# Kernel optimization log

Measured on AMD Instinct MI355X. Metric: run time of the kernel, lower is better.

Reference implementation:

```python
import jax, jax.numpy as jnp
import numpy as np

N_NODES = 50000
N_EDGES = 800000
D = 64  # node_dim == edge_dim
NEG_SLOPE = 0.2
EPS = 1e-5


def _lin_params(key, d_in, d_out):
    k1, k2 = jax.random.split(key)
    bound = 1.0 / np.sqrt(d_in)
    W = jax.random.uniform(k1, (d_out, d_in), minval=-bound, maxval=bound, dtype=jnp.float32)
    b = jax.random.uniform(k2, (d_out,), minval=-bound, maxval=bound, dtype=jnp.float32)
    return W, b


def setup_inputs() -> dict:
    key = jax.random.key(0)
    ks = jax.random.split(key, 12)
    V = jax.random.normal(ks[0], (N_NODES, D), dtype=jnp.float32)
    E = jax.random.normal(ks[1], (N_EDGES, D), dtype=jnp.float32)
    src = jax.random.randint(ks[2], (N_EDGES,), 0, N_NODES, dtype=jnp.int32)
    dst = jax.random.randint(ks[3], (N_EDGES,), 0, N_NODES, dtype=jnp.int32)
    pA_w, pA_b = _lin_params(ks[4], D, D)   # NodePooling.A
    pB_w, pB_b = _lin_params(ks[5], D, D)   # NodePooling.B
    mW1, mb1 = _lin_params(ks[6], D, D)     # edge MLP layer 1
    mW2, mb2 = _lin_params(ks[7], D, D)     # edge MLP layer 2
    BW, Bb = _lin_params(ks[8], D, D)       # GenMessage.B (scale)
    CW, Cb = _lin_params(ks[9], D, D)       # GenMessage.C (shift)
    return {"V": V, "E": E, "src": src, "dst": dst,
            "pA_w": pA_w, "pA_b": pA_b, "pB_w": pB_w, "pB_b": pB_b,
            "mW1": mW1, "mb1": mb1, "mW2": mW2, "mb2": mb2,
            "BW": BW, "Bb": Bb, "CW": CW, "Cb": Cb}


def _lrelu(x):
    return jnp.where(x >= 0, x, NEG_SLOPE * x)


def reference(V, E, src, dst, pA_w, pA_b, pB_w, pB_b, mW1, mb1, mW2, mb2, BW, Bb, CW, Cb):
    n = V.shape[0]
    # V = act(V); NodePooling: B(lrelu(A(V)))
    Va = _lrelu(V)
    Vp = _lrelu(Va @ pA_w.T + pA_b) @ pB_w.T + pB_b  # [N, D]
    # edge MLP on edge features (2 Linear+ReLU layers)
    x = jax.nn.relu(E @ mW1.T + mb1)
    x = jax.nn.relu(x @ mW2.T + mb2)                  # [E, D]
    scale = jax.nn.sigmoid(x @ BW.T + Bb)
    shift = x @ CW.T + Cb
    # gathered src features, gated affine message
    M1 = scale * Vp[src] + shift                      # [E, D]
    M2 = M1 * M1
    # segment-mean onto dst (DGL fn.mean); zero for isolated nodes
    deg = jax.ops.segment_sum(jnp.ones((dst.shape[0],), jnp.float32), dst, num_segments=n)
    denom = jnp.maximum(deg, 1.0)[:, None]
    V1 = jax.ops.segment_sum(M1, dst, num_segments=n) / denom
    V2 = jax.ops.segment_sum(M2, dst, num_segments=n) / denom
    return jnp.sqrt(jax.nn.relu(V2 - V1) + EPS)
```

## Files before the change

kernel.cpp:

```cpp
#include <hip/hip_runtime.h>

#define NN 50000
#define NE 800000
#define DDIM 64
#define PADX 68
#define PADS 68
#define NB_SCAN ((NN + 255) / 256)
#define NPB ((NN + 63) / 64)
#define NEG_SLOPE 0.2f
#define EPS_V 1e-5f

typedef short bf16x8 __attribute__((ext_vector_type(8)));
typedef float f32x4 __attribute__((ext_vector_type(4)));

__device__ __forceinline__ float lrelu_f(float x) { return x >= 0.0f ? x : NEG_SLOPE * x; }

__device__ __forceinline__ unsigned short bf16_rn(float x) {
    union { float f; unsigned int u; } c; c.f = x;
    unsigned int r = c.u + 0x7FFF + ((c.u >> 16) & 1);
    return (unsigned short)(r >> 16);
}
__device__ __forceinline__ float bf16_tof(unsigned short h) {
    union { float f; unsigned int u; } c; c.u = ((unsigned int)h) << 16;
    return c.f;
}

__device__ __forceinline__ unsigned cvtpk_bf16(float a, float b) {
    unsigned r;
    asm("v_cvt_pk_bf16_f32 %0, %1, %2" : "=v"(r) : "v"(a), "v"(b));
    return r;
}

__device__ __forceinline__ void split8(const float* __restrict__ v, bf16x8& h, bf16x8& l)
{
    union { bf16x8 v8; unsigned u[4]; } H, L;
    #pragma unroll
    for (int k = 0; k < 4; ++k) {
        float a = v[2*k], b = v[2*k+1];
        unsigned p = cvtpk_bf16(a, b);
        union { float f; unsigned u; } h0, h1;
        h0.u = p << 16;
        h1.u = p & 0xFFFF0000u;
        unsigned q = cvtpk_bf16(a - h0.f, b - h1.f);
        H.u[k] = p;
        L.u[k] = q;
    }
    h = H.v8; l = L.v8;
}

__device__ __forceinline__ void mma_tile(float acc[16], const float* __restrict__ XT,
                                         const float* __restrict__ Wc, int e0, int f0)
{
    #pragma unroll 4
    for (int kk = 0; kk < DDIM; kk += 4) {
        float4 A0 = *(const float4*)&XT[(kk+0)*PADX + e0];
        float4 A1 = *(const float4*)&XT[(kk+1)*PADX + e0];
        float4 A2 = *(const float4*)&XT[(kk+2)*PADX + e0];
        float4 A3 = *(const float4*)&XT[(kk+3)*PADX + e0];
        float4 B0 = *(const float4*)&Wc[(f0+0)*PADX + kk];
        float4 B1 = *(const float4*)&Wc[(f0+1)*PADX + kk];
        float4 B2 = *(const float4*)&Wc[(f0+2)*PADX + kk];
        float4 B3 = *(const float4*)&Wc[(f0+3)*PADX + kk];
        const float a[4][4] = {{A0.x,A0.y,A0.z,A0.w},{A1.x,A1.y,A1.z,A1.w},
                               {A2.x,A2.y,A2.z,A2.w},{A3.x,A3.y,A3.z,A3.w}};
        const float b[4][4] = {{B0.x,B0.y,B0.z,B0.w},{B1.x,B1.y,B1.z,B1.w},
                               {B2.x,B2.y,B2.z,B2.w},{B3.x,B3.y,B3.z,B3.w}};
        #pragma unroll
        for (int j = 0; j < 4; ++j)
            #pragma unroll
            for (int i = 0; i < 4; ++i)
                #pragma unroll
                for (int q = 0; q < 4; ++q)
                    acc[i*4+j] = fmaf(a[q][i], b[j][q], acc[i*4+j]);
    }
}

__device__ __forceinline__ void load_w_f32(float* __restrict__ Wc, const float* __restrict__ Wg, int tid)
{
    #pragma unroll
    for (int c = 0; c < 4; ++c) {
        int idx = (c << 10) + (tid << 2);
        int f = idx >> 6, k = idx & 63;
        *(float4*)&Wc[f*PADX + k] = *(const float4*)&Wg[idx];
    }
}

__global__ __launch_bounds__(256, 3)
void node_pool_kernel(const float* __restrict__ V,
                      const float* __restrict__ Aw, const float* __restrict__ Ab,
                      const float* __restrict__ Bw, const float* __restrict__ Bbv,
                      float* __restrict__ Vp,
                      const int* __restrict__ dst, int* __restrict__ degi,
                      const float* __restrict__ W1, const float* __restrict__ W2,
                      const float* __restrict__ WB, const float* __restrict__ WC,
                      short* __restrict__ WF)
{
    __shared__ float Wc[DDIM*PADX];
    __shared__ float XT[DDIM*PADX];
    const int tid = threadIdx.x;

    if (blockIdx.x >= NPB) {
        int gid = (blockIdx.x - NPB) * 256 + tid;
        int L = gid >> 12, r = gid & 4095;
        int t = r >> 10, ks = (r >> 9) & 1, lane = (r >> 3) & 63, j = r & 7;
        const float* Ws = (L == 0) ? W1 : (L == 1) ? W2 : (L == 2) ? WB : WC;
        int n = lane & 15, kg = lane >> 4;
        int f = t*16 + n, k = ks*32 + kg*8 + j;
        float v = Ws[f*64 + k];
        unsigned short h = bf16_rn(v);
        unsigned short l = bf16_rn(v - bf16_tof(h));
        int base = L*8192 + ((t*2 + ks)*2)*512 + lane*8 + j;
        WF[base]       = (short)h;
        WF[base + 512] = (short)l;

        const int stride = gridDim.x * 256;
        for (int e = blockIdx.x * 256 + tid; e < NE; e += stride)
            atomicAdd(&degi[dst[e]], 1);
        return;
    }

    const int nb = blockIdx.x * 64;
    const int e0 = (tid & 15) << 2;
    const int f0 = (tid >> 4) << 2;

    #pragma unroll
    for (int c = 0; c < 4; ++c) {
        int idx = (c << 10) + (tid << 2);
        int e = idx >> 6, d = idx & 63;
        int row = nb + e; if (row > NN-1) row = NN-1;
        float4 v = *(const float4*)&V[(size_t)row*DDIM + d];
        XT[(d+0)*PADX + e] = lrelu_f(v.x);
        XT[(d+1)*PADX + e] = lrelu_f(v.y);
        XT[(d+2)*PADX + e] = lrelu_f(v.z);
        XT[(d+3)*PADX + e] = lrelu_f(v.w);
    }
    load_w_f32(Wc, Aw, tid);
    __syncthreads();

    float acc[16];
    #pragma unroll
    for (int i = 0; i < 16; ++i) acc[i] = 0.f;
    mma_tile(acc, XT, Wc, e0, f0);
    __syncthreads();

    {
        float4 bv = *(const float4*)&Ab[f0];
        const float ba[4] = {bv.x, bv.y, bv.z, bv.w};
        #pragma unroll
        for (int j = 0; j < 4; ++j) {
            float4 v;
            v.x = lrelu_f(acc[0*4+j] + ba[j]);
            v.y = lrelu_f(acc[1*4+j] + ba[j]);
            v.z = lrelu_f(acc[2*4+j] + ba[j]);
            v.w = lrelu_f(acc[3*4+j] + ba[j]);
            *(float4*)&XT[(f0+j)*PADX + e0] = v;
        }
    }
    load_w_f32(Wc, Bw, tid);
    __syncthreads();

    float acc2[16];
    #pragma unroll
    for (int i = 0; i < 16; ++i) acc2[i] = 0.f;
    mma_tile(acc2, XT, Wc, e0, f0);

    float4 bv = *(const float4*)&Bbv[f0];
    #pragma unroll
    for (int i = 0; i < 4; ++i) {
        int row = nb + e0 + i;
        if (row < NN) {
            float4 o;
            o.x = acc2[i*4+0] + bv.x;
            o.y = acc2[i*4+1] + bv.y;
            o.z = acc2[i*4+2] + bv.z;
            o.w = acc2[i*4+3] + bv.w;
            *(float4*)&Vp[(size_t)row*DDIM + f0] = o;
        }
    }

    const int stride = gridDim.x * 256;
    for (int e = blockIdx.x * 256 + tid; e < NE; e += stride)
        atomicAdd(&degi[dst[e]], 1);
}

__global__ __launch_bounds__(256)
void csr_build_kernel(const int* __restrict__ degi, int* __restrict__ linc,
                      int* __restrict__ bsum, int* __restrict__ curs,
                      const int* __restrict__ dst, int* __restrict__ eidx,
                      float* __restrict__ Szero,
                      int* __restrict__ bar)
{
    __shared__ int ws[4];
    __shared__ int base_s;
    const int tid = threadIdx.x;
    const int lane = tid & 63, wv = tid >> 6;
    const int gstride = NB_SCAN * 256;

    {
        float4 z = {0.f, 0.f, 0.f, 0.f};
        float4* p = (float4*)Szero;
        const int total = 2 * NN * DDIM / 4;
        for (int i = blockIdx.x * 256 + tid; i < total; i += gstride)
            p[i] = z;
    }

    const int i = blockIdx.x * 256 + tid;
    const int dv = (i < NN) ? degi[i] : 0;
    {
        int sc = dv;
        #pragma unroll
        for (int off = 1; off < 64; off <<= 1) {
            int t = __shfl_up(sc, off, 64);
            if (lane >= off) sc += t;
        }
        if (lane == 63) ws[wv] = sc;
        __syncthreads();
        int wb = 0;
        #pragma unroll
        for (int w = 0; w < 4; ++w) if (w < wv) wb += ws[w];
        int incl = sc + wb;
        if (i < NN) linc[i] = incl;
        if (tid == 255) atomicExch(&bsum[blockIdx.x], incl);
    }

    __syncthreads();
    if (tid == 0) {
        __threadfence();
        atomicAdd(&bar[0], 1);
        while (atomicAdd(&bar[0], 0) < NB_SCAN) ;
        __threadfence();
    }
    __syncthreads();

    {
        int v2 = (tid < NB_SCAN) ? atomicAdd(&bsum[tid], 0) : 0;
        int sc2 = v2;
        #pragma unroll
        for (int off = 1; off < 64; off <<= 1) {
            int t = __shfl_up(sc2, off, 64);
            if (lane >= off) sc2 += t;
        }
        if (lane == 63) ws[wv] = sc2;
        __syncthreads();
        int wb2 = 0;
        #pragma unroll
        for (int w = 0; w < 4; ++w) if (w < wv) wb2 += ws[w];
        if (tid == blockIdx.x) base_s = sc2 + wb2 - v2;
        __syncthreads();
        if (i < NN) atomicExch(&curs[i], base_s + linc[i] - dv);
    }

    __syncthreads();
    if (tid == 0) {
        __threadfence();
        atomicAdd(&bar[1], 1);
        while (atomicAdd(&bar[1], 0) < NB_SCAN) ;
        __threadfence();
    }
    __syncthreads();

    for (int e = blockIdx.x * 256 + tid; e < NE; e += gstride) {
        int p = atomicAdd(&curs[dst[e]], 1);
        eidx[p] = e;
    }
}

__device__ __forceinline__ void gemm64_dual_lds(const short* bw, int lane,
                                                const bf16x8 ah0[2], const bf16x8 al0[2],
                                                const bf16x8 ah1[2], const bf16x8 al1[2],
                                                f32x4 acc0[4], f32x4 acc1[4])
{
    #pragma unroll
    for (int ks = 0; ks < 2; ++ks) {
        bf16x8 bh[4], bl[4];
        #pragma unroll
        for (int t = 0; t < 4; ++t) {
            bh[t] = *(const bf16x8*)&bw[(((t*2 + ks)*2 + 0)*64 + lane)*8];
            bl[t] = *(const bf16x8*)&bw[(((t*2 + ks)*2 + 1)*64 + lane)*8];
        }
        #pragma unroll
        for (int t = 0; t < 4; ++t) {
            acc0[t] = __builtin_amdgcn_mfma_f32_16x16x32_bf16(al0[ks], bh[t], acc0[t], 0, 0, 0);
            acc1[t] = __builtin_amdgcn_mfma_f32_16x16x32_bf16(al1[ks], bh[t], acc1[t], 0, 0, 0);
            acc0[t] = __builtin_amdgcn_mfma_f32_16x16x32_bf16(ah0[ks], bl[t], acc0[t], 0, 0, 0);
            acc1[t] = __builtin_amdgcn_mfma_f32_16x16x32_bf16(ah1[ks], bl[t], acc1[t], 0, 0, 0);
            acc0[t] = __builtin_amdgcn_mfma_f32_16x16x32_bf16(ah0[ks], bh[t], acc0[t], 0, 0, 0);
            acc1[t] = __builtin_amdgcn_mfma_f32_16x16x32_bf16(ah1[ks], bh[t], acc1[t], 0, 0, 0);
        }
    }
}

__device__ __forceinline__ void transpose_frags(float* __restrict__ sw, const f32x4 y[4],
                                                int lane, bf16x8 ah[2], bf16x8 al[2])
{
    const int n = lane & 15, mg = lane >> 4;
    #pragma unroll
    for (int t = 0; t < 4; ++t)
        #pragma unroll
        for (int r = 0; r < 4; ++r)
            sw[(mg*4 + r)*PADS + t*16 + n] = y[t][r];
    __builtin_amdgcn_wave_barrier();
    const int m = lane & 15, kg = lane >> 4;
    float x[16];
    *(float4*)&x[0]  = *(const float4*)&sw[m*PADS + kg*8];
    *(float4*)&x[4]  = *(const float4*)&sw[m*PADS + kg*8 + 4];
    *(float4*)&x[8]  = *(const float4*)&sw[m*PADS + 32 + kg*8];
    *(float4*)&x[12] = *(const float4*)&sw[m*PADS + 32 + kg*8 + 4];
    split8(&x[0], ah[0], al[0]);
    split8(&x[8], ah[1], al[1]);
    __builtin_amdgcn_wave_barrier();
}

__global__ __launch_bounds__(256, 3)
void edge_fused_kernel(const float* __restrict__ Eg,
                       const int* __restrict__ src, const int* __restrict__ dst,
                       const int* __restrict__ eidx,
                       const short* __restrict__ WF,
                       const float* __restrict__ b1, const float* __restrict__ b2,
                       const float* __restrict__ bB, const float* __restrict__ bC,
                       const float* __restrict__ Vp,
                       float* __restrict__ S1, float* __restrict__ S2)
{
    __shared__ __align__(16) short bw[8192];
    __shared__ float scratch[4 * 16 * PADS];
    __shared__ int aux[4 * 64];

    const int tid = threadIdx.x;
    const int lane = tid & 63, wv = tid >> 6;
    float* sw = scratch + wv * 16 * PADS;
    int* auxw = aux + wv * 64;

    const int ew = blockIdx.x * 128 + wv * 32;
    const int m = lane & 15, kg = lane >> 4;
    const int n = lane & 15, mg = lane >> 4;

    uint4 w0, w1, w2, w3;
    #define ISSUE_W(Wg) do { const uint4* s_ = (const uint4*)(Wg); \
        w0 = s_[tid]; w1 = s_[256 + tid]; w2 = s_[512 + tid]; w3 = s_[768 + tid]; } while (0)
    #define COMMIT_W() do { __syncthreads(); uint4* d_ = (uint4*)bw; \
        d_[tid] = w0; d_[256 + tid] = w1; d_[512 + tid] = w2; d_[768 + tid] = w3; \
        __syncthreads(); } while (0)

    ISSUE_W(WF);

    if (lane < 32) {
        int eg = eidx[ew + lane];
        auxw[lane]      = src[eg];
        auxw[32 + lane] = dst[eg];
    }
    bf16x8 ah0[2], al0[2], ah1[2], al1[2];
    {
        int eg0 = eidx[ew + m];
        int eg1 = eidx[ew + 16 + m];
        const float* er0 = Eg + (size_t)eg0*DDIM + kg*8;
        const float* er1 = Eg + (size_t)eg1*DDIM + kg*8;
        float x[16];
        *(float4*)&x[0]  = *(const float4*)&er0[0];
        *(float4*)&x[4]  = *(const float4*)&er0[4];
        *(float4*)&x[8]  = *(const float4*)&er0[32];
        *(float4*)&x[12] = *(const float4*)&er0[36];
        split8(&x[0], ah0[0], al0[0]);
        split8(&x[8], ah0[1], al0[1]);
        *(float4*)&x[0]  = *(const float4*)&er1[0];
        *(float4*)&x[4]  = *(const float4*)&er1[4];
        *(float4*)&x[8]  = *(const float4*)&er1[32];
        *(float4*)&x[12] = *(const float4*)&er1[36];
        split8(&x[0], ah1[0], al1[0]);
        split8(&x[8], ah1[1], al1[1]);
    }

    COMMIT_W();
    ISSUE_W(WF + 8192);
    f32x4 acc0[4], acc1[4];
    #pragma unroll
    for (int t = 0; t < 4; ++t) { acc0[t] = (f32x4){0.f,0.f,0.f,0.f}; acc1[t] = (f32x4){0.f,0.f,0.f,0.f}; }
    __builtin_amdgcn_s_setprio(1);
    gemm64_dual_lds(bw, lane, ah0, al0, ah1, al1, acc0, acc1);
    __builtin_amdgcn_s_setprio(0);
    #pragma unroll
    for (int t = 0; t < 4; ++t) {
        float b = b1[t*16 + n];
        #pragma unroll
        for (int r = 0; r < 4; ++r) {
            acc0[t][r] = fmaxf(acc0[t][r] + b, 0.0f);
            acc1[t][r] = fmaxf(acc1[t][r] + b, 0.0f);
        }
    }
    transpose_frags(sw, acc0, lane, ah0, al0);
    transpose_frags(sw, acc1, lane, ah1, al1);

    COMMIT_W();
    ISSUE_W(WF + 2*8192);
    #pragma unroll
    for (int t = 0; t < 4; ++t) { acc0[t] = (f32x4){0.f,0.f,0.f,0.f}; acc1[t] = (f32x4){0.f,0.f,0.f,0.f}; }
    __builtin_amdgcn_s_setprio(1);
    gemm64_dual_lds(bw, lane, ah0, al0, ah1, al1, acc0, acc1);
    __builtin_amdgcn_s_setprio(0);
    #pragma unroll
    for (int t = 0; t < 4; ++t) {
        float b = b2[t*16 + n];
        #pragma unroll
        for (int r = 0; r < 4; ++r) {
            acc0[t][r] = fmaxf(acc0[t][r] + b, 0.0f);
            acc1[t][r] = fmaxf(acc1[t][r] + b, 0.0f);
        }
    }
    transpose_frags(sw, acc0, lane, ah0, al0);
    transpose_frags(sw, acc1, lane, ah1, al1);

    COMMIT_W();
    ISSUE_W(WF + 3*8192);
    f32x4 accS0[4], accS1[4];
    #pragma unroll
    for (int t = 0; t < 4; ++t) { accS0[t] = (f32x4){0.f,0.f,0.f,0.f}; accS1[t] = (f32x4){0.f,0.f,0.f,0.f}; }
    __builtin_amdgcn_s_setprio(1);
    gemm64_dual_lds(bw, lane, ah0, al0, ah1, al1, accS0, accS1);
    __builtin_amdgcn_s_setprio(0);

    COMMIT_W();
    f32x4 accH0[4], accH1[4];
    #pragma unroll
    for (int t = 0; t < 4; ++t) { accH0[t] = (f32x4){0.f,0.f,0.f,0.f}; accH1[t] = (f32x4){0.f,0.f,0.f,0.f}; }
    __builtin_amdgcn_s_setprio(1);
    gemm64_dual_lds(bw, lane, ah0, al0, ah1, al1, accH0, accH1);
    __builtin_amdgcn_s_setprio(0);

    const int f = lane;
    float s1 = 0.f, s2 = 0.f;
    int prev = auxw[32];
    #pragma unroll
    for (int tile = 0; tile < 2; ++tile) {
        const int to = tile * 16;
        f32x4* accS = tile ? accS1 : accS0;
        f32x4* accH = tile ? accH1 : accH0;

        {
            int sn[4];
            #pragma unroll
            for (int r = 0; r < 4; ++r) sn[r] = auxw[to + mg*4 + r];
            #pragma unroll
            for (int t = 0; t < 4; ++t) {
                const int ff = t*16 + n;
                const float bBv = bB[ff];
                const float bCv = bC[ff];
                #pragma unroll
                for (int r = 0; r < 4; ++r) {
                    float vp = Vp[(size_t)sn[r]*DDIM + ff];
                    float sg = 1.0f / (1.0f + __expf(-(accS[t][r] + bBv)));
                    sw[(mg*4 + r)*PADS + ff] = fmaf(sg, vp, accH[t][r] + bCv);
                }
            }
        }
        __builtin_amdgcn_wave_barrier();

        #pragma unroll 4
        for (int e = 0; e < 16; ++e) {
            int dn = auxw[32 + to + e];
            float m1 = sw[e*PADS + f];
            float m2 = m1 * m1;
            if (dn != prev) {
                atomicAdd(&S1[(size_t)prev*DDIM + f], s1);
                atomicAdd(&S2[(size_t)prev*DDIM + f], s2);
                s1 = 0.f; s2 = 0.f; prev = dn;
            }
            s1 += m1; s2 += m2;
        }
        __builtin_amdgcn_wave_barrier();
    }
    atomicAdd(&S1[(size_t)prev*DDIM + f], s1);
    atomicAdd(&S2[(size_t)prev*DDIM + f], s2);
    #undef ISSUE_W
    #undef COMMIT_W
}

__global__ __launch_bounds__(256)
void finalize_kernel(const float* __restrict__ S1, const float* __restrict__ S2,
                     const int* __restrict__ degi, float* __restrict__ out)
{
    int gid = blockIdx.x * blockDim.x + threadIdx.x;
    if (gid >= NN*DDIM) return;
    int n = gid >> 6;
    float dn = (float)degi[n];
    dn = dn > 1.0f ? dn : 1.0f;
    float v = (S2[gid] - S1[gid]) / dn;
    out[gid] = sqrtf(fmaxf(v, 0.0f) + EPS_V);
}

extern "C" void kernel_launch(void* const* d_in, const int* in_sizes, int n_in,
                              void* d_out, int out_size, void* d_ws, size_t ws_size,
                              hipStream_t stream) {
    const float* V   = (const float*)d_in[0];
    const float* Eg  = (const float*)d_in[1];
    const int*   src = (const int*)d_in[2];
    const int*   dst = (const int*)d_in[3];
    const float* pAw = (const float*)d_in[4];
    const float* pAb = (const float*)d_in[5];
    const float* pBw = (const float*)d_in[6];
    const float* pBb = (const float*)d_in[7];
    const float* mW1 = (const float*)d_in[8];
    const float* mb1 = (const float*)d_in[9];
    const float* mW2 = (const float*)d_in[10];
    const float* mb2 = (const float*)d_in[11];
    const float* BW  = (const float*)d_in[12];
    const float* Bb  = (const float*)d_in[13];
    const float* CW  = (const float*)d_in[14];
    const float* Cb  = (const float*)d_in[15];
    float* out = (float*)d_out;

    float* ws    = (float*)d_ws;
    float* Vp    = ws;
    float* S1    = ws + (size_t)NN*DDIM;
    float* S2    = ws + (size_t)2*NN*DDIM;
    int*   degi  = (int*)(ws + (size_t)3*NN*DDIM);
    int*   curs  = degi + NN;
    int*   linc  = curs + NN;
    int*   bsum  = linc + NN;
    int*   bar   = bsum + NB_SCAN;
    int*   eidx  = bar + 2;
    short* WF    = (short*)(eidx + NE);

    hipMemsetAsync(degi, 0, (size_t)(3*NN + NB_SCAN + 2) * sizeof(int), stream);

    node_pool_kernel<<<NPB + 64, 256, 0, stream>>>(V, pAw, pAb, pBw, pBb, Vp, dst, degi,
                                                   mW1, mW2, BW, CW, WF);
    csr_build_kernel<<<NB_SCAN, 256, 0, stream>>>(degi, linc, bsum, curs, dst, eidx,
                                                  S1, bar);
    edge_fused_kernel<<<NE/128, 256, 0, stream>>>(Eg, src, dst, eidx, WF,
                                                  mb1, mb2, Bb, Cb, Vp, S1, S2);
    finalize_kernel<<<(NN*DDIM + 255)/256, 256, 0, stream>>>(S1, S2, degi, out);
}
```

Measured before the change: 504.5 us.

## Split CSR build into scan and wide scatter kernels, memset accumulators

The single 196-block CSR build kernel, which zeroed the S1/S2 accumulators, scanned degrees, spun on a second grid barrier and then scattered edge indices, is split up. The zeroing moves into one larger hipMemsetAsync. The scan keeps one grid barrier and drops the linc buffer. The edge scatter becomes its own kernel launched with one thread per edge for full-GPU parallelism. This removes a spin barrier and gives the scatter and zeroing far more parallelism, at the cost of one extra kernel launch.

```diff
diff --git a/kernel.cpp b/kernel.cpp
--- a/kernel.cpp
+++ b/kernel.cpp
@@ -184,28 +184,17 @@
 }
 
 __global__ __launch_bounds__(256)
-void csr_build_kernel(const int* __restrict__ degi, int* __restrict__ linc,
-                      int* __restrict__ bsum, int* __restrict__ curs,
-                      const int* __restrict__ dst, int* __restrict__ eidx,
-                      float* __restrict__ Szero,
-                      int* __restrict__ bar)
+void scan_fused_kernel(const int* __restrict__ degi, int* __restrict__ bsum,
+                       int* __restrict__ curs, int* __restrict__ bar)
 {
     __shared__ int ws[4];
     __shared__ int base_s;
     const int tid = threadIdx.x;
     const int lane = tid & 63, wv = tid >> 6;
-    const int gstride = NB_SCAN * 256;
-
-    {
-        float4 z = {0.f, 0.f, 0.f, 0.f};
-        float4* p = (float4*)Szero;
-        const int total = 2 * NN * DDIM / 4;
-        for (int i = blockIdx.x * 256 + tid; i < total; i += gstride)
-            p[i] = z;
-    }
-
     const int i = blockIdx.x * 256 + tid;
     const int dv = (i < NN) ? degi[i] : 0;
+
+    int incl;
     {
         int sc = dv;
         #pragma unroll
@@ -218,8 +207,7 @@
         int wb = 0;
         #pragma unroll
         for (int w = 0; w < 4; ++w) if (w < wv) wb += ws[w];
-        int incl = sc + wb;
-        if (i < NN) linc[i] = incl;
+        incl = sc + wb;
         if (tid == 255) atomicExch(&bsum[blockIdx.x], incl);
     }
 
@@ -247,20 +235,16 @@
         for (int w = 0; w < 4; ++w) if (w < wv) wb2 += ws[w];
         if (tid == blockIdx.x) base_s = sc2 + wb2 - v2;
         __syncthreads();
-        if (i < NN) atomicExch(&curs[i], base_s + linc[i] - dv);
-    }
-
-    __syncthreads();
-    if (tid == 0) {
-        __threadfence();
-        atomicAdd(&bar[1], 1);
-        while (atomicAdd(&bar[1], 0) < NB_SCAN) ;
-        __threadfence();
-    }
-    __syncthreads();
-
-    for (int e = blockIdx.x * 256 + tid; e < NE; e += gstride) {
-        int p = atomicAdd(&curs[dst[e]], 1);
+        if (i < NN) curs[i] = base_s + incl - dv;
+    }
+}
+
+__global__ __launch_bounds__(256)
+void scatter_kernel(const int* __restrict__ dst, int* __restrict__ cursor, int* __restrict__ eidx)
+{
+    int e = blockIdx.x * 256 + threadIdx.x;
+    if (e < NE) {
+        int p = atomicAdd(&cursor[dst[e]], 1);
         eidx[p] = e;
     }
 }
@@ -513,18 +497,17 @@
     float* S2    = ws + (size_t)2*NN*DDIM;
     int*   degi  = (int*)(ws + (size_t)3*NN*DDIM);
     int*   curs  = degi + NN;
-    int*   linc  = curs + NN;
-    int*   bsum  = linc + NN;
+    int*   bsum  = curs + NN;
     int*   bar   = bsum + NB_SCAN;
     int*   eidx  = bar + 2;
     short* WF    = (short*)(eidx + NE);
 
-    hipMemsetAsync(degi, 0, (size_t)(3*NN + NB_SCAN + 2) * sizeof(int), stream);
+    hipMemsetAsync(S1, 0, ((size_t)2*NN*DDIM + 2*NN + NB_SCAN + 2) * sizeof(float), stream);
 
     node_pool_kernel<<<NPB + 64, 256, 0, stream>>>(V, pAw, pAb, pBw, pBb, Vp, dst, degi,
                                                    mW1, mW2, BW, CW, WF);
-    csr_build_kernel<<<NB_SCAN, 256, 0, stream>>>(degi, linc, bsum, curs, dst, eidx,
-                                                  S1, bar);
+    scan_fused_kernel<<<NB_SCAN, 256, 0, stream>>>(degi, bsum, curs, bar);
+    scatter_kernel<<<(NE + 255)/256, 256, 0, stream>>>(dst, curs, eidx);
     edge_fused_kernel<<<NE/128, 256, 0, stream>>>(Eg, src, dst, eidx, WF,
                                                   mb1, mb2, Bb, Cb, Vp, S1, S2);
     finalize_kernel<<<(NN*DDIM + 255)/256, 256, 0, stream>>>(S1, S2, degi, out);
```

After: 494.1 us. 1.02x faster.
